# Kernel tuning notes

Hardware: AMD Instinct MI355X
Metric: run time of the kernel (lower is better)

## Reference

```python
import jax, jax.numpy as jnp
import numpy as np

N, E, B = 24000, 96000, 1200
NPG = N // B  # nodes per graph

def _lin(k, fi, fo):
    s = 1.0 / np.sqrt(fi)
    return jax.random.uniform(k, (fi, fo), jnp.float32, -s, s)

def setup_inputs():
    key = jax.random.key(0)
    ks = jax.random.split(key, 32)
    x = jax.random.normal(ks[0], (N, 9), jnp.float32)
    edge_attr = jax.random.normal(ks[1], (E, 4), jnp.float32)
    src = jax.random.randint(ks[2], (E,), 0, N)
    # destination node within the same graph as the source (block-diagonal adjacency)
    dst = (src // NPG) * NPG + jax.random.randint(ks[3], (E,), 0, NPG)
    edge_index = jnp.stack([src, dst]).astype(jnp.int32)
    batch = (jnp.arange(N) // NPG).astype(jnp.int32)
    fp_batch = jax.random.normal(ks[4], (B, 2048), jnp.float32)
    p = dict(
        Wq1=_lin(ks[5], 9, 512), bq1=jnp.zeros(512, jnp.float32),
        Wk1=_lin(ks[6], 9, 512), bk1=jnp.zeros(512, jnp.float32),
        Wv1=_lin(ks[7], 9, 512), bv1=jnp.zeros(512, jnp.float32),
        We1=_lin(ks[8], 4, 512),
        Ws1=_lin(ks[9], 9, 512), bs1=jnp.zeros(512, jnp.float32),
        Wq2=_lin(ks[10], 512, 1024), bq2=jnp.zeros(1024, jnp.float32),
        Wk2=_lin(ks[11], 512, 1024), bk2=jnp.zeros(1024, jnp.float32),
        Wv2=_lin(ks[12], 512, 1024), bv2=jnp.zeros(1024, jnp.float32),
        We2=_lin(ks[13], 4, 1024),
        Ws2=_lin(ks[14], 512, 1024), bs2=jnp.zeros(1024, jnp.float32),
        Wfp=_lin(ks[15], 2048, 256), bfp=jnp.zeros(256, jnp.float32),
        Wfin=_lin(ks[16], 1280, 1024), bfin=jnp.zeros(1024, jnp.float32),
    )
    return dict(x=x, edge_index=edge_index, edge_attr=edge_attr, batch=batch, fp_batch=fp_batch, **p)

def _tconv(x, src, dst, ea, Wq, bq, Wk, bk, Wv, bv, We, Ws, bs, H, C):
    """PyG TransformerConv: concat=True, beta=False, root_weight=True."""
    n = x.shape[0]
    q = (x @ Wq + bq).reshape(n, H, C)
    k = (x @ Wk + bk).reshape(n, H, C)
    v = (x @ Wv + bv).reshape(n, H, C)
    e = (ea @ We).reshape(-1, H, C)            # lin_edge has no bias
    ke = k[src] + e                            # [E,H,C]
    alpha = jnp.einsum('ehc,ehc->eh', q[dst], ke) / jnp.sqrt(jnp.float32(C))
    # scatter-softmax over incoming edges of each target node
    amax = jax.ops.segment_max(alpha, dst, num_segments=n)
    amax = jnp.where(jnp.isfinite(amax), amax, 0.0)  # nodes with no in-edges
    ex = jnp.exp(alpha - amax[dst])
    den = jax.ops.segment_sum(ex, dst, num_segments=n)[dst] + 1e-16
    msg = (v[src] + e) * (ex / den)[:, :, None]
    out = jax.ops.segment_sum(msg, dst, num_segments=n).reshape(n, H * C)
    return out + x @ Ws + bs                   # root/skip connection

def reference(x, edge_index, edge_attr, batch, fp_batch, Wq1, bq1, Wk1, bk1, Wv1, bv1, We1, Ws1, bs1, Wq2, bq2, Wk2, bk2, Wv2, bv2, We2, Ws2, bs2, Wfp, bfp, Wfin, bfin):
    src, dst = edge_index[0], edge_index[1]
    h = jax.nn.relu(_tconv(x, src, dst, edge_attr, Wq1, bq1, Wk1, bk1, Wv1, bv1, We1, Ws1, bs1, 4, 128))
    h = _tconv(h, src, dst, edge_attr, Wq2, bq2, Wk2, bk2, Wv2, bv2, We2, Ws2, bs2, 4, 256)
    cnt = jax.ops.segment_sum(jnp.ones((h.shape[0],), h.dtype), batch, num_segments=B)
    g = jax.ops.segment_sum(h, batch, num_segments=B) / cnt[:, None]  # global_mean_pool
    fp = fp_batch @ Wfp + bfp
    return jnp.concatenate([g, fp], axis=-1) @ Wfin + bfin
```

## Files before the change

kernel.cpp:

```cpp
#include <hip/hip_runtime.h>
#include <cstdint>
#include <cstddef>

static constexpr int NN = 24000;
static constexpr int NE = 96000;
static constexpr int NB = 1200;
static constexpr int NPG = 20;
static constexpr int MPAD = 24064;

typedef __attribute__((ext_vector_type(8))) short bfv8;
typedef __attribute__((ext_vector_type(4))) float fv4;

__device__ __forceinline__ unsigned f2ord(float f){
  unsigned u = __float_as_uint(f);
  return (u & 0x80000000u) ? ~u : (u | 0x80000000u);
}
__device__ __forceinline__ float ord2f(unsigned u){
  return (u & 0x80000000u) ? __uint_as_float(u & 0x7FFFFFFFu)
                           : __uint_as_float(~u);
}
__device__ __forceinline__ unsigned short f2bf(float f){
  unsigned u = __float_as_uint(f);
  u += 0x7FFFu + ((u >> 16) & 1u);
  return (unsigned short)(u >> 16);
}
__device__ __forceinline__ float bf2f(unsigned short s){
  return __uint_as_float(((unsigned)s) << 16);
}

__global__ __launch_bounds__(256) void count_kernel(const int* __restrict__ dst,
                                                    unsigned* __restrict__ deg)
{
  int e = blockIdx.x*256 + threadIdx.x;
  if (e < NE) atomicAdd(&deg[dst[e]], 1u);
}

__global__ __launch_bounds__(1024) void scan_kernel(const unsigned* __restrict__ deg,
                                                    unsigned* __restrict__ rowstart)
{
  __shared__ unsigned s[1024];
  __shared__ unsigned carry_s;
  int tid = threadIdx.x;
  if (tid == 0) carry_s = 0;
  __syncthreads();
  for (int base = 0; base < NN; base += 1024){
    unsigned v = (base + tid < NN) ? deg[base + tid] : 0u;
    s[tid] = v;
    __syncthreads();
#pragma unroll
    for (int off = 1; off < 1024; off <<= 1){
      unsigned t = (tid >= off) ? s[tid - off] : 0u;
      __syncthreads();
      s[tid] += t;
      __syncthreads();
    }
    unsigned carry = carry_s;
    if (base + tid < NN) rowstart[base + tid] = carry + s[tid] - v;
    __syncthreads();
    if (tid == 0) carry_s = carry + s[1023];
    __syncthreads();
  }
  if (tid == 0) rowstart[NN] = carry_s;
}

__global__ __launch_bounds__(256) void scatter_kernel(const int* __restrict__ dst,
                                                      const unsigned* __restrict__ rowstart,
                                                      unsigned* __restrict__ cur,
                                                      int* __restrict__ eidx)
{
  int e = blockIdx.x*256 + threadIdx.x;
  if (e >= NE) return;
  int d = dst[e];
  unsigned p = rowstart[d] + atomicAdd(&cur[d], 1u);
  eidx[p] = e;
}

template<bool BA, bool BB>
__global__ __launch_bounds__(256) void node_gemm_l1_pair(
    const float* __restrict__ x,
    const float* __restrict__ Wa, const float* __restrict__ ba,
    const float* __restrict__ Wb, const float* __restrict__ bb,
    void* __restrict__ outa, void* __restrict__ outb)
{
  int t = blockIdx.x*256 + threadIdx.x;
  if (t >= NN*512) return;
  int n = t >> 9, j = t & 511;
  float xr[9];
#pragma unroll
  for (int i=0;i<9;i++) xr[i] = x[n*9+i];
  float aa=ba[j], ab=bb[j];
#pragma unroll
  for (int i=0;i<9;i++){
    float xi = xr[i];
    aa += xi*Wa[i*512+j];
    ab += xi*Wb[i*512+j];
  }
  if (BA) ((unsigned short*)outa)[t] = f2bf(aa); else ((float*)outa)[t] = aa;
  if (BB) ((unsigned short*)outb)[t] = f2bf(ab); else ((float*)outb)[t] = ab;
}

__global__ __launch_bounds__(256) void alpha_bf16_hc512(
    const unsigned short* __restrict__ q, const unsigned short* __restrict__ k,
    const float* __restrict__ ea, const float* __restrict__ We,
    const int* __restrict__ src, const int* __restrict__ dst,
    const int* __restrict__ eidx,
    float* __restrict__ alpha, unsigned* __restrict__ amax)
{
  int wave = (blockIdx.x*256 + threadIdx.x) >> 6;
  int lane = threadIdx.x & 63;
  if (wave >= NE) return;
  int e = eidx[wave];
  int s = src[e], d = dst[e];
  float ea0=ea[e*4+0], ea1=ea[e*4+1], ea2=ea[e*4+2], ea3=ea[e*4+3];
  const float scale = 0.088388347648318447f;
  int off = lane*8;
  bfv8 qv = *reinterpret_cast<const bfv8*>(q + (size_t)d*512 + off);
  bfv8 kv = *reinterpret_cast<const bfv8*>(k + (size_t)s*512 + off);
  float part = 0.f;
#pragma unroll
  for (int j=0;j<8;j++){
    int f = off + j;
    float ef = ea0*We[f] + ea1*We[512+f] + ea2*We[1024+f] + ea3*We[1536+f];
    part += bf2f((unsigned short)qv[j]) * (bf2f((unsigned short)kv[j]) + ef);
  }
#pragma unroll
  for (int o=8; o>=1; o>>=1) part += __shfl_xor(part, o);
  if ((lane & 15) == 0){
    int h = lane >> 4;
    float a = part*scale;
    alpha[e*4+h] = a;
    atomicMax(&amax[d*4+h], f2ord(a));
  }
}

__global__ __launch_bounds__(256) void alpha_bf16_hc1024(
    const unsigned short* __restrict__ q, const unsigned short* __restrict__ k,
    const float* __restrict__ ea, const float* __restrict__ We,
    const int* __restrict__ src, const int* __restrict__ dst,
    const int* __restrict__ eidx,
    float* __restrict__ alpha, unsigned* __restrict__ amax)
{
  int wave = (blockIdx.x*256 + threadIdx.x) >> 6;
  int lane = threadIdx.x & 63;
  if (wave >= NE) return;
  int e = eidx[wave];
  int s = src[e], d = dst[e];
  float ea0=ea[e*4+0], ea1=ea[e*4+1], ea2=ea[e*4+2], ea3=ea[e*4+3];
  const float scale = 1.0f/16.0f;
#pragma unroll
  for (int p=0;p<2;p++){
    int off = p*512 + lane*8;
    bfv8 qv = *reinterpret_cast<const bfv8*>(q + (size_t)d*1024 + off);
    bfv8 kv = *reinterpret_cast<const bfv8*>(k + (size_t)s*1024 + off);
    float part = 0.f;
#pragma unroll
    for (int j=0;j<8;j++){
      int f = off + j;
      float ef = ea0*We[f] + ea1*We[1024+f] + ea2*We[2048+f] + ea3*We[3072+f];
      part += bf2f((unsigned short)qv[j]) * (bf2f((unsigned short)kv[j]) + ef);
    }
#pragma unroll
    for (int o=16; o>=1; o>>=1) part += __shfl_xor(part, o);
    if ((lane & 31) == 0){
      int h = p*2 + (lane>>5);
      float a = part*scale;
      alpha[e*4+h] = a;
      atomicMax(&amax[d*4+h], f2ord(a));
    }
  }
}

__global__ __launch_bounds__(256) void ex_kernel(
    float* __restrict__ alpha, const unsigned* __restrict__ amax,
    const int* __restrict__ dst, float* __restrict__ den)
{
  int t = blockIdx.x*256 + threadIdx.x;
  if (t >= NE*4) return;
  int e = t>>2, h = t&3;
  int d = dst[e];
  float m = ord2f(amax[d*4+h]);
  float v = __expf(alpha[t]-m);
  alpha[t] = v;
  unsafeAtomicAdd(&den[d*4+h], v);
}

__global__ __launch_bounds__(256) void gather512_kernel(
    const unsigned short* __restrict__ v, const float* __restrict__ ea,
    const float* __restrict__ We,
    const int* __restrict__ src,
    const unsigned* __restrict__ rowstart, const int* __restrict__ eidx,
    const float* __restrict__ exw, const float* __restrict__ den,
    const unsigned short* __restrict__ accin, unsigned short* __restrict__ hb)
{
  int n = blockIdx.x;
  int tid = threadIdx.x;
  int h = tid >> 6;
  int f2 = tid*2;
  unsigned p0 = rowstart[n], p1 = rowstart[n+1];
  float2 W0 = *reinterpret_cast<const float2*>(We + 0*512 + f2);
  float2 W1 = *reinterpret_cast<const float2*>(We + 1*512 + f2);
  float2 W2 = *reinterpret_cast<const float2*>(We + 2*512 + f2);
  float2 W3 = *reinterpret_cast<const float2*>(We + 3*512 + f2);
  float rdn = 1.0f / (den[n*4+h] + 1e-16f);
  ushort2 a0 = *reinterpret_cast<const ushort2*>(accin + (size_t)n*512 + f2);
  float2 s = make_float2(bf2f(a0.x), bf2f(a0.y));
  for (unsigned p = p0; p < p1; ++p){
    int e  = eidx[p];
    float w = exw[e*4+h] * rdn;
    float4 eav = *reinterpret_cast<const float4*>(ea + (size_t)e*4);
    ushort2 vv = *reinterpret_cast<const ushort2*>(v + (size_t)src[e]*512 + f2);
    float efx = eav.x*W0.x + eav.y*W1.x + eav.z*W2.x + eav.w*W3.x;
    float efy = eav.x*W0.y + eav.y*W1.y + eav.z*W2.y + eav.w*W3.y;
    s.x += w*(bf2f(vv.x) + efx);
    s.y += w*(bf2f(vv.y) + efy);
  }
  ushort2 o;
  o.x = f2bf(fmaxf(s.x, 0.0f));
  o.y = f2bf(fmaxf(s.y, 0.0f));
  *reinterpret_cast<ushort2*>(hb + (size_t)n*512 + f2) = o;
}

__global__ __launch_bounds__(256) void gather1024_kernel(
    const unsigned short* __restrict__ v, const float* __restrict__ ea,
    const float* __restrict__ We,
    const int* __restrict__ src,
    const unsigned* __restrict__ rowstart, const int* __restrict__ eidx,
    const float* __restrict__ exw, const float* __restrict__ den,
    unsigned short* __restrict__ acc)
{
  int n = blockIdx.x;
  int tid = threadIdx.x;
  int h = tid >> 6;
  int f4 = tid*4;
  unsigned p0 = rowstart[n], p1 = rowstart[n+1];
  float4 W0 = *reinterpret_cast<const float4*>(We + 0*1024 + f4);
  float4 W1 = *reinterpret_cast<const float4*>(We + 1*1024 + f4);
  float4 W2 = *reinterpret_cast<const float4*>(We + 2*1024 + f4);
  float4 W3 = *reinterpret_cast<const float4*>(We + 3*1024 + f4);
  float rdn = 1.0f / (den[n*4+h] + 1e-16f);
  ushort4 a0 = *reinterpret_cast<const ushort4*>(acc + (size_t)n*1024 + f4);
  float4 s = make_float4(bf2f(a0.x), bf2f(a0.y), bf2f(a0.z), bf2f(a0.w));
  for (unsigned p = p0; p < p1; ++p){
    int e  = eidx[p];
    float w = exw[e*4+h] * rdn;
    float4 eav = *reinterpret_cast<const float4*>(ea + (size_t)e*4);
    ushort4 vv = *reinterpret_cast<const ushort4*>(v + (size_t)src[e]*1024 + f4);
    s.x += w*(bf2f(vv.x) + eav.x*W0.x + eav.y*W1.x + eav.z*W2.x + eav.w*W3.x);
    s.y += w*(bf2f(vv.y) + eav.x*W0.y + eav.y*W1.y + eav.z*W2.y + eav.w*W3.y);
    s.z += w*(bf2f(vv.z) + eav.x*W0.z + eav.y*W1.z + eav.z*W2.z + eav.w*W3.z);
    s.w += w*(bf2f(vv.w) + eav.x*W0.w + eav.y*W1.w + eav.z*W2.w + eav.w*W3.w);
  }
  ushort4 o;
  o.x = f2bf(s.x); o.y = f2bf(s.y); o.z = f2bf(s.z); o.w = f2bf(s.w);
  *reinterpret_cast<ushort4*>(acc + (size_t)n*1024 + f4) = o;
}

__global__ __launch_bounds__(256) void cvt_wt_kernel(const float* __restrict__ W,
                                                     unsigned short* __restrict__ Wt)
{
  int t = blockIdx.x*256 + threadIdx.x;
  if (t >= 1024*512) return;
  int n = t >> 9, k = t & 511;
  Wt[t] = f2bf(W[k*1024 + n]);
}

template<bool BOUT>
__global__ __launch_bounds__(256) void gemm_bf16_mfma(
    const unsigned short* __restrict__ A,
    const unsigned short* __restrict__ B,
    const float* __restrict__ bias,
    void* __restrict__ Cout, int M)
{
  constexpr int K = 512, N = 1024;
  __shared__ unsigned short As[128*32];
  __shared__ unsigned short Bs[128*32];
  int tid  = threadIdx.x;
  int wid  = tid >> 6, lane = tid & 63;
  int wr   = wid >> 1, wc = wid & 1;
  int bm   = blockIdx.y * 128, bn = blockIdx.x * 128;
  int l15  = lane & 15, kg = lane >> 4;

  int r0 = (wid*2+0)*16 + (lane>>2);
  int r1 = (wid*2+1)*16 + (lane>>2);
  int s0 = lane & 3;
  int kc0 = s0 ^ ((r0>>1)&3);
  int kc1 = s0 ^ ((r1>>1)&3);
  unsigned short* ldsA0 = As + (wid*2+0)*512;
  unsigned short* ldsA1 = As + (wid*2+1)*512;
  unsigned short* ldsB0 = Bs + (wid*2+0)*512;
  unsigned short* ldsB1 = Bs + (wid*2+1)*512;

  fv4 acc[4][4];
#pragma unroll
  for (int m=0;m<4;m++)
#pragma unroll
    for (int n=0;n<4;n++) acc[m][n] = (fv4){0.f,0.f,0.f,0.f};

  for (int k0 = 0; k0 < K; k0 += 32){
    __syncthreads();
    __builtin_amdgcn_global_load_lds(
        (const __attribute__((address_space(1))) void*)(A + (size_t)(bm+r0)*K + k0 + kc0*8),
        (__attribute__((address_space(3))) void*)ldsA0, 16, 0, 0);
    __builtin_amdgcn_global_load_lds(
        (const __attribute__((address_space(1))) void*)(A + (size_t)(bm+r1)*K + k0 + kc1*8),
        (__attribute__((address_space(3))) void*)ldsA1, 16, 0, 0);
    __builtin_amdgcn_global_load_lds(
        (const __attribute__((address_space(1))) void*)(B + (size_t)(bn+r0)*K + k0 + kc0*8),
        (__attribute__((address_space(3))) void*)ldsB0, 16, 0, 0);
    __builtin_amdgcn_global_load_lds(
        (const __attribute__((address_space(1))) void*)(B + (size_t)(bn+r1)*K + k0 + kc1*8),
        (__attribute__((address_space(3))) void*)ldsB1, 16, 0, 0);
    __syncthreads();
    bfv8 af[4], bfr[4];
#pragma unroll
    for (int m=0;m<4;m++){
      int r  = wr*64 + m*16 + l15;
      int sl = kg ^ ((r>>1)&3);
      af[m] = *reinterpret_cast<const bfv8*>(reinterpret_cast<char*>(As) + r*64 + sl*16);
    }
#pragma unroll
    for (int n=0;n<4;n++){
      int r  = wc*64 + n*16 + l15;
      int sl = kg ^ ((r>>1)&3);
      bfr[n] = *reinterpret_cast<const bfv8*>(reinterpret_cast<char*>(Bs) + r*64 + sl*16);
    }
#pragma unroll
    for (int m=0;m<4;m++)
#pragma unroll
      for (int n=0;n<4;n++)
        acc[m][n] = __builtin_amdgcn_mfma_f32_16x16x32_bf16(af[m], bfr[n], acc[m][n], 0, 0, 0);
  }
#pragma unroll
  for (int m=0;m<4;m++){
#pragma unroll
    for (int n=0;n<4;n++){
      int col = bn + wc*64 + n*16 + l15;
      float bcol = bias[col];
#pragma unroll
      for (int r=0;r<4;r++){
        int row = bm + wr*64 + m*16 + (lane>>4)*4 + r;
        if (row < M){
          float val = acc[m][n][r] + bcol;
          if (BOUT) ((unsigned short*)Cout)[(size_t)row*N + col] = f2bf(val);
          else      ((float*)Cout)[(size_t)row*N + col] = val;
        }
      }
    }
  }
}

__global__ __launch_bounds__(256) void sgemm_partial(
    const float* __restrict__ A, const float* __restrict__ W,
    float* __restrict__ P, int M, int N, int K, int kchunk, int zoff)
{
  __shared__ float As[32][68];
  __shared__ __align__(16) float Bs[32][64];
  int tid = threadIdx.x;
  int bm = blockIdx.y*64, bn = blockIdx.x*64;
  int kbeg = blockIdx.z*kchunk;
  int kend = min(kbeg + kchunk, K);
  float* Pz = P + (size_t)(zoff + blockIdx.z)*M*N;
  int ty = tid >> 4, tx = tid & 15;
  float acc[4][4] = {};
  for (int k0 = kbeg; k0 < kend; k0 += 32){
#pragma unroll
    for (int i=0;i<2;i++){
      int lin = tid + i*256;
      int r = lin >> 3;
      int kq = (lin & 7) * 4;
      float4 av = make_float4(0.f,0.f,0.f,0.f);
      int row = bm + r;
      if (row < M) av = *reinterpret_cast<const float4*>(A + (size_t)row*K + k0 + kq);
      As[kq+0][r]=av.x; As[kq+1][r]=av.y; As[kq+2][r]=av.z; As[kq+3][r]=av.w;
    }
#pragma unroll
    for (int i=0;i<2;i++){
      int lin = tid + i*256;
      int kr = lin >> 4;
      int c4 = (lin & 15) * 4;
      float4 wv = *reinterpret_cast<const float4*>(W + (size_t)(k0+kr)*N + bn + c4);
      *reinterpret_cast<float4*>(&Bs[kr][c4]) = wv;
    }
    __syncthreads();
#pragma unroll
    for (int kk=0;kk<32;kk++){
      float a[4], b[4];
#pragma unroll
      for (int i=0;i<4;i++) a[i] = As[kk][ty*4+i];
#pragma unroll
      for (int j=0;j<4;j++) b[j] = Bs[kk][tx*4+j];
#pragma unroll
      for (int i=0;i<4;i++)
#pragma unroll
        for (int j=0;j<4;j++) acc[i][j] += a[i]*b[j];
    }
    __syncthreads();
  }
#pragma unroll
  for (int i=0;i<4;i++){
    int row = bm + ty*4 + i;
    if (row >= M) break;
#pragma unroll
    for (int j=0;j<4;j++)
      Pz[(size_t)row*N + bn + tx*4 + j] = acc[i][j];
  }
}

__global__ __launch_bounds__(256) void reduce_add_kernel(
    const float* __restrict__ P, const float* __restrict__ bias,
    float* __restrict__ O, int total, int nz, int nmask)
{
  int t = blockIdx.x*256 + threadIdx.x;
  if (t >= total) return;
  float s = bias[t & nmask];
  for (int z = 0; z < nz; ++z) s += P[(size_t)z*total + t];
  O[t] = s;
}

__global__ __launch_bounds__(256) void pool_kernel(const unsigned short* __restrict__ h2,
                                                   float* __restrict__ g)
{
  int t = blockIdx.x*256 + threadIdx.x;
  if (t >= NB*256) return;
  int b = t >> 8, f4 = (t & 255) * 4;
  float4 s = make_float4(0.f,0.f,0.f,0.f);
#pragma unroll
  for (int i=0;i<NPG;i++){
    ushort4 v = *reinterpret_cast<const ushort4*>(h2 + (size_t)(b*NPG+i)*1024 + f4);
    s.x += bf2f(v.x); s.y += bf2f(v.y); s.z += bf2f(v.z); s.w += bf2f(v.w);
  }
  s.x *= (1.0f/NPG); s.y *= (1.0f/NPG); s.z *= (1.0f/NPG); s.w *= (1.0f/NPG);
  *reinterpret_cast<float4*>(g + (size_t)b*1024 + f4) = s;
}

extern "C" void kernel_launch(void* const* d_in, const int* in_sizes, int n_in,
                              void* d_out, int out_size, void* d_ws, size_t ws_size,
                              hipStream_t stream)
{
  const float* x    = (const float*)d_in[0];
  const int*   ei   = (const int*)d_in[1];
  const float* ea   = (const float*)d_in[2];
  const float* fpb  = (const float*)d_in[4];
  const float* Wq1  = (const float*)d_in[5];  const float* bq1 = (const float*)d_in[6];
  const float* Wk1  = (const float*)d_in[7];  const float* bk1 = (const float*)d_in[8];
  const float* Wv1  = (const float*)d_in[9];  const float* bv1 = (const float*)d_in[10];
  const float* We1  = (const float*)d_in[11];
  const float* Ws1  = (const float*)d_in[12]; const float* bs1 = (const float*)d_in[13];
  const float* Wq2  = (const float*)d_in[14]; const float* bq2 = (const float*)d_in[15];
  const float* Wk2  = (const float*)d_in[16]; const float* bk2 = (const float*)d_in[17];
  const float* Wv2  = (const float*)d_in[18]; const float* bv2 = (const float*)d_in[19];
  const float* We2  = (const float*)d_in[20];
  const float* Ws2  = (const float*)d_in[21]; const float* bs2 = (const float*)d_in[22];
  const float* Wfp  = (const float*)d_in[23]; const float* bfp = (const float*)d_in[24];
  const float* Wfin = (const float*)d_in[25]; const float* bfin= (const float*)d_in[26];
  const int* src = ei;
  const int* dst = ei + NE;
  float* out = (float*)d_out;

  const size_t F512  = (size_t)NN*512;
  const size_t F1024 = (size_t)NN*1024;
  float* base = (float*)d_ws;
  float* C_a = base;
  float* C_b = base + F1024;
  float* H   = base + 2*F1024;
  unsigned short* q1b = (unsigned short*)C_a;
  unsigned short* v1b = (unsigned short*)C_a;
  unsigned short* k1b = (unsigned short*)H;
  unsigned short* s1b = (unsigned short*)H;
  unsigned short* hb  = (unsigned short*)C_a + F1024;
  unsigned short* q2b = (unsigned short*)C_a;
  unsigned short* k2b = (unsigned short*)C_b;
  unsigned short* v2b = (unsigned short*)C_a;
  unsigned short* s2b = (unsigned short*)C_b;
  unsigned short* WtQ = (unsigned short*)H;
  unsigned short* WtK = WtQ + (size_t)1024*512;
  unsigned short* WtV = WtK + (size_t)1024*512;
  unsigned short* WtS = WtV + (size_t)1024*512;
  float* P1 = C_a;
  float* P2 = C_a + 5*(size_t)NB*1024;

  float* tail = base + 2*F1024 + F512;
  float*    alphab   = tail;
  unsigned* amax     = (unsigned*)(alphab + (size_t)NE*4);
  float*    den      = (float*)(amax + (size_t)NN*4);
  unsigned* deg      = (unsigned*)(den + (size_t)NN*4);
  unsigned* cur      = deg + NN;
  unsigned* rowstart = cur + NN;
  int*      eidx     = (int*)(rowstart + NN + 1);
  float*    g        = (float*)(eidx + NE);
  float*    fp       = g + (size_t)NB*1024;

  hipMemsetAsync(deg, 0, sizeof(unsigned)*NN, stream);
  hipMemsetAsync(cur, 0, sizeof(unsigned)*NN, stream);
  count_kernel<<<(NE+255)/256, 256, 0, stream>>>(dst, deg);
  scan_kernel<<<1, 1024, 0, stream>>>(deg, rowstart);
  scatter_kernel<<<(NE+255)/256, 256, 0, stream>>>(dst, rowstart, cur, eidx);

  hipMemsetAsync(amax, 0, sizeof(unsigned)*(size_t)NN*4, stream);
  hipMemsetAsync(den,  0, sizeof(float)*(size_t)NN*4, stream);

  node_gemm_l1_pair<true,true><<<(NN*512+255)/256, 256, 0, stream>>>(
      x, Wq1,bq1, Wk1,bk1, q1b, k1b);
  alpha_bf16_hc512<<<NE/4, 256, 0, stream>>>(q1b, k1b, ea, We1, src, dst, eidx,
                                             alphab, amax);
  ex_kernel<<<(NE*4+255)/256, 256, 0, stream>>>(alphab, amax, dst, den);
  node_gemm_l1_pair<true,true><<<(NN*512+255)/256, 256, 0, stream>>>(
      x, Wv1,bv1, Ws1,bs1, v1b, s1b);
  gather512_kernel<<<NN, 256, 0, stream>>>(v1b, ea, We1, src, rowstart, eidx,
                                           alphab, den, s1b, hb);
  hipMemsetAsync(hb + F512, 0, (size_t)(MPAD-NN)*512*sizeof(unsigned short), stream);

  cvt_wt_kernel<<<(1024*512+255)/256, 256, 0, stream>>>(Wq2, WtQ);
  cvt_wt_kernel<<<(1024*512+255)/256, 256, 0, stream>>>(Wk2, WtK);
  cvt_wt_kernel<<<(1024*512+255)/256, 256, 0, stream>>>(Wv2, WtV);
  cvt_wt_kernel<<<(1024*512+255)/256, 256, 0, stream>>>(Ws2, WtS);

  hipMemsetAsync(amax, 0, sizeof(unsigned)*(size_t)NN*4, stream);
  hipMemsetAsync(den,  0, sizeof(float)*(size_t)NN*4, stream);

  {
    dim3 grid(8, MPAD/128);
    gemm_bf16_mfma<true><<<grid, 256, 0, stream>>>(hb, WtQ, bq2, q2b, NN);
    gemm_bf16_mfma<true><<<grid, 256, 0, stream>>>(hb, WtK, bk2, k2b, NN);
  }
  alpha_bf16_hc1024<<<NE/4, 256, 0, stream>>>(q2b, k2b, ea, We2, src, dst, eidx,
                                              alphab, amax);
  ex_kernel<<<(NE*4+255)/256, 256, 0, stream>>>(alphab, amax, dst, den);
  {
    dim3 grid(8, MPAD/128);
    gemm_bf16_mfma<true><<<grid, 256, 0, stream>>>(hb, WtV, bv2, v2b, NN);
    gemm_bf16_mfma<true><<<grid, 256, 0, stream>>>(hb, WtS, bs2, s2b, NN);
  }
  gather1024_kernel<<<NN, 256, 0, stream>>>(v2b, ea, We2, src, rowstart, eidx,
                                            alphab, den, s2b);

  pool_kernel<<<(NB*256+255)/256, 256, 0, stream>>>(s2b, g);

  {
    dim3 gfp(256/64, (NB+63)/64, 8);
    sgemm_partial<<<gfp, 256, 0, stream>>>(fpb, Wfp, P2, NB, 256, 2048, 256, 0);
    reduce_add_kernel<<<(NB*256+255)/256, 256, 0, stream>>>(P2, bfp, fp, NB*256, 8, 255);
  }
  {
    dim3 g1(1024/64, (NB+63)/64, 4);
    sgemm_partial<<<g1, 256, 0, stream>>>(g, Wfin, P1, NB, 1024, 1024, 256, 0);
    dim3 g2(1024/64, (NB+63)/64, 1);
    sgemm_partial<<<g2, 256, 0, stream>>>(fp, Wfin + (size_t)1024*1024, P1, NB, 1024, 256, 256, 4);
    reduce_add_kernel<<<(NB*1024+255)/256, 256, 0, stream>>>(P1, bfin, out, NB*1024, 5, 1023);
  }
}
```

Before: 821.2 us.

## Precompute per-node q·We projection to drop edge-term from alpha kernels

Rewrites the q·(k+e) attention score as q·k plus ea·(q·We per head), where the per-node projection q·We is computed once per node through precomputed Wq·We and bq·We matrices. The alpha kernels no longer rebuild the edge embedding per feature per edge, which removes many We loads and FMAs from the per-edge inner loop. This adds small precompute kernels and a per-node projection pass. The projection uses fp32 weights instead of the bf16-rounded q, so numerics shift slightly.

```diff
diff --git a/kernel.cpp b/kernel.cpp
--- a/kernel.cpp
+++ b/kernel.cpp
@@ -99,9 +99,95 @@
   if (BB) ((unsigned short*)outb)[t] = f2bf(ab); else ((float*)outb)[t] = ab;
 }
 
+__global__ __launch_bounds__(256) void make_wt1_kernel(
+    const float* __restrict__ Wq1, const float* __restrict__ bq1,
+    const float* __restrict__ We1, float* __restrict__ WT1, float* __restrict__ tb1)
+{
+  int t = threadIdx.x;
+  if (t < 144){
+    int m = t >> 4, idx = t & 15, h = idx >> 2, c = idx & 3;
+    int f0 = h*128;
+    float s = 0.f;
+    for (int j=0;j<128;j++) s += Wq1[m*512 + f0+j] * We1[c*512 + f0+j];
+    WT1[m*16 + idx] = s;
+  } else if (t < 160){
+    int idx = t - 144, h = idx >> 2, c = idx & 3;
+    int f0 = h*128;
+    float s = 0.f;
+    for (int j=0;j<128;j++) s += bq1[f0+j] * We1[c*512 + f0+j];
+    tb1[idx] = s;
+  }
+}
+
+__global__ __launch_bounds__(256) void make_wt2_kernel(
+    const float* __restrict__ Wq2, const float* __restrict__ bq2,
+    const float* __restrict__ We2, float* __restrict__ WT2, float* __restrict__ tb2)
+{
+  int t = blockIdx.x*256 + threadIdx.x;
+  if (t < 8192){
+    int m = t >> 4, idx = t & 15, h = idx >> 2, c = idx & 3;
+    int f0 = h*256;
+    float s = 0.f;
+    for (int j=0;j<256;j++) s += Wq2[m*1024 + f0+j] * We2[c*1024 + f0+j];
+    WT2[m*16 + idx] = s;
+  } else if (t < 8208){
+    int idx = t - 8192, h = idx >> 2, c = idx & 3;
+    int f0 = h*256;
+    float s = 0.f;
+    for (int j=0;j<256;j++) s += bq2[f0+j] * We2[c*1024 + f0+j];
+    tb2[idx] = s;
+  }
+}
+
+__global__ __launch_bounds__(256) void tproj1_kernel(
+    const float* __restrict__ x, const float* __restrict__ WT1,
+    const float* __restrict__ tb1, float* __restrict__ tp)
+{
+  int t = blockIdx.x*256 + threadIdx.x;
+  if (t >= NN*16) return;
+  int n = t >> 4, idx = t & 15;
+  float s = tb1[idx];
+#pragma unroll
+  for (int i=0;i<9;i++) s += x[n*9+i] * WT1[i*16 + idx];
+  tp[t] = s;
+}
+
+__global__ __launch_bounds__(256) void tproj2_kernel(
+    const unsigned short* __restrict__ hb, const float* __restrict__ WT2,
+    const float* __restrict__ tb2, float* __restrict__ tp)
+{
+  int wave = (blockIdx.x*256 + threadIdx.x) >> 6;
+  int lane = threadIdx.x & 63;
+  if (wave >= NN) return;
+  int p = lane & 15, g = lane >> 4;
+  int c4 = g*4;
+  int m0 = p*32;
+  float4 acc = make_float4(0.f,0.f,0.f,0.f);
+#pragma unroll
+  for (int b=0;b<4;b++){
+    bfv8 hv = *reinterpret_cast<const bfv8*>(hb + (size_t)wave*512 + m0 + b*8);
+#pragma unroll
+    for (int j=0;j<8;j++){
+      float hf = bf2f((unsigned short)hv[j]);
+      float4 w = *reinterpret_cast<const float4*>(WT2 + (m0 + b*8 + j)*16 + c4);
+      acc.x += hf*w.x; acc.y += hf*w.y; acc.z += hf*w.z; acc.w += hf*w.w;
+    }
+  }
+#pragma unroll
+  for (int o=8;o>=1;o>>=1){
+    acc.x += __shfl_xor(acc.x,o); acc.y += __shfl_xor(acc.y,o);
+    acc.z += __shfl_xor(acc.z,o); acc.w += __shfl_xor(acc.w,o);
+  }
+  if (p == 0){
+    float4 tb = *reinterpret_cast<const float4*>(tb2 + c4);
+    float4 o4 = make_float4(acc.x+tb.x, acc.y+tb.y, acc.z+tb.z, acc.w+tb.w);
+    *reinterpret_cast<float4*>(tp + (size_t)wave*16 + c4) = o4;
+  }
+}
+
 __global__ __launch_bounds__(256) void alpha_bf16_hc512(
     const unsigned short* __restrict__ q, const unsigned short* __restrict__ k,
-    const float* __restrict__ ea, const float* __restrict__ We,
+    const float* __restrict__ ea, const float* __restrict__ tp,
     const int* __restrict__ src, const int* __restrict__ dst,
     const int* __restrict__ eidx,
     float* __restrict__ alpha, unsigned* __restrict__ amax)
@@ -111,23 +197,21 @@
   if (wave >= NE) return;
   int e = eidx[wave];
   int s = src[e], d = dst[e];
-  float ea0=ea[e*4+0], ea1=ea[e*4+1], ea2=ea[e*4+2], ea3=ea[e*4+3];
   const float scale = 0.088388347648318447f;
   int off = lane*8;
   bfv8 qv = *reinterpret_cast<const bfv8*>(q + (size_t)d*512 + off);
   bfv8 kv = *reinterpret_cast<const bfv8*>(k + (size_t)s*512 + off);
   float part = 0.f;
 #pragma unroll
-  for (int j=0;j<8;j++){
-    int f = off + j;
-    float ef = ea0*We[f] + ea1*We[512+f] + ea2*We[1024+f] + ea3*We[1536+f];
-    part += bf2f((unsigned short)qv[j]) * (bf2f((unsigned short)kv[j]) + ef);
-  }
+  for (int j=0;j<8;j++)
+    part += bf2f((unsigned short)qv[j]) * bf2f((unsigned short)kv[j]);
 #pragma unroll
   for (int o=8; o>=1; o>>=1) part += __shfl_xor(part, o);
   if ((lane & 15) == 0){
     int h = lane >> 4;
-    float a = part*scale;
+    float4 tv  = *reinterpret_cast<const float4*>(tp + (size_t)d*16 + h*4);
+    float4 eav = *reinterpret_cast<const float4*>(ea + (size_t)e*4);
+    float a = (part + eav.x*tv.x + eav.y*tv.y + eav.z*tv.z + eav.w*tv.w)*scale;
     alpha[e*4+h] = a;
     atomicMax(&amax[d*4+h], f2ord(a));
   }
@@ -135,7 +219,7 @@
 
 __global__ __launch_bounds__(256) void alpha_bf16_hc1024(
     const unsigned short* __restrict__ q, const unsigned short* __restrict__ k,
-    const float* __restrict__ ea, const float* __restrict__ We,
+    const float* __restrict__ ea, const float* __restrict__ tp,
     const int* __restrict__ src, const int* __restrict__ dst,
     const int* __restrict__ eidx,
     float* __restrict__ alpha, unsigned* __restrict__ amax)
@@ -145,7 +229,6 @@
   if (wave >= NE) return;
   int e = eidx[wave];
   int s = src[e], d = dst[e];
-  float ea0=ea[e*4+0], ea1=ea[e*4+1], ea2=ea[e*4+2], ea3=ea[e*4+3];
   const float scale = 1.0f/16.0f;
 #pragma unroll
   for (int p=0;p<2;p++){
@@ -154,16 +237,15 @@
     bfv8 kv = *reinterpret_cast<const bfv8*>(k + (size_t)s*1024 + off);
     float part = 0.f;
 #pragma unroll
-    for (int j=0;j<8;j++){
-      int f = off + j;
-      float ef = ea0*We[f] + ea1*We[1024+f] + ea2*We[2048+f] + ea3*We[3072+f];
-      part += bf2f((unsigned short)qv[j]) * (bf2f((unsigned short)kv[j]) + ef);
-    }
+    for (int j=0;j<8;j++)
+      part += bf2f((unsigned short)qv[j]) * bf2f((unsigned short)kv[j]);
 #pragma unroll
     for (int o=16; o>=1; o>>=1) part += __shfl_xor(part, o);
     if ((lane & 31) == 0){
       int h = p*2 + (lane>>5);
-      float a = part*scale;
+      float4 tv  = *reinterpret_cast<const float4*>(tp + (size_t)d*16 + h*4);
+      float4 eav = *reinterpret_cast<const float4*>(ea + (size_t)e*4);
+      float a = (part + eav.x*tv.x + eav.y*tv.y + eav.z*tv.z + eav.w*tv.w)*scale;
       alpha[e*4+h] = a;
       atomicMax(&amax[d*4+h], f2ord(a));
     }
@@ -489,19 +571,27 @@
   int*      eidx     = (int*)(rowstart + NN + 1);
   float*    g        = (float*)(eidx + NE);
   float*    fp       = g + (size_t)NB*1024;
+  float*    tproj    = fp + (size_t)NB*256;
+  float*    WT2b     = tproj + (size_t)NN*16;
+  float*    tb2b     = WT2b + 8192;
+  float*    WT1b     = tb2b + 16;
+  float*    tb1b     = WT1b + 144;
 
   hipMemsetAsync(deg, 0, sizeof(unsigned)*NN, stream);
   hipMemsetAsync(cur, 0, sizeof(unsigned)*NN, stream);
   count_kernel<<<(NE+255)/256, 256, 0, stream>>>(dst, deg);
   scan_kernel<<<1, 1024, 0, stream>>>(deg, rowstart);
   scatter_kernel<<<(NE+255)/256, 256, 0, stream>>>(dst, rowstart, cur, eidx);
+  make_wt1_kernel<<<1, 256, 0, stream>>>(Wq1, bq1, We1, WT1b, tb1b);
+  make_wt2_kernel<<<33, 256, 0, stream>>>(Wq2, bq2, We2, WT2b, tb2b);
+  tproj1_kernel<<<(NN*16+255)/256, 256, 0, stream>>>(x, WT1b, tb1b, tproj);
 
   hipMemsetAsync(amax, 0, sizeof(unsigned)*(size_t)NN*4, stream);
   hipMemsetAsync(den,  0, sizeof(float)*(size_t)NN*4, stream);
 
   node_gemm_l1_pair<true,true><<<(NN*512+255)/256, 256, 0, stream>>>(
       x, Wq1,bq1, Wk1,bk1, q1b, k1b);
-  alpha_bf16_hc512<<<NE/4, 256, 0, stream>>>(q1b, k1b, ea, We1, src, dst, eidx,
+  alpha_bf16_hc512<<<NE/4, 256, 0, stream>>>(q1b, k1b, ea, tproj, src, dst, eidx,
                                              alphab, amax);
   ex_kernel<<<(NE*4+255)/256, 256, 0, stream>>>(alphab, amax, dst, den);
   node_gemm_l1_pair<true,true><<<(NN*512+255)/256, 256, 0, stream>>>(
@@ -514,6 +604,7 @@
   cvt_wt_kernel<<<(1024*512+255)/256, 256, 0, stream>>>(Wk2, WtK);
   cvt_wt_kernel<<<(1024*512+255)/256, 256, 0, stream>>>(Wv2, WtV);
   cvt_wt_kernel<<<(1024*512+255)/256, 256, 0, stream>>>(Ws2, WtS);
+  tproj2_kernel<<<(NN*64+255)/256, 256, 0, stream>>>(hb, WT2b, tb2b, tproj);
 
   hipMemsetAsync(amax, 0, sizeof(unsigned)*(size_t)NN*4, stream);
   hipMemsetAsync(den,  0, sizeof(float)*(size_t)NN*4, stream);
@@ -523,7 +614,7 @@
     gemm_bf16_mfma<true><<<grid, 256, 0, stream>>>(hb, WtQ, bq2, q2b, NN);
     gemm_bf16_mfma<true><<<grid, 256, 0, stream>>>(hb, WtK, bk2, k2b, NN);
   }
-  alpha_bf16_hc1024<<<NE/4, 256, 0, stream>>>(q2b, k2b, ea, We2, src, dst, eidx,
+  alpha_bf16_hc1024<<<NE/4, 256, 0, stream>>>(q2b, k2b, ea, tproj, src, dst, eidx,
                                               alphab, amax);
   ex_kernel<<<(NE*4+255)/256, 256, 0, stream>>>(alphab, amax, dst, den);
   {
```

Measured after the change: 903.6 us. 10.0% more time.
